# Performance work log

Hardware: AMD Instinct MI355X
Metric: run time of the kernel (lower is better)

## Reference

```python
import jax, jax.numpy as jnp
import numpy as np

B, S, T = 64, 128, 64
V, E, H, L = 32000, 512, 512, 2
PAD, BOS = 0, 1


def setup_inputs() -> dict:
    key = jax.random.key(0)
    ks = jax.random.split(key, 14)
    w = lambda k, shape: (jax.random.normal(k, shape, jnp.float32) * 0.05)
    src_emb = w(ks[0], (V, E)).at[PAD].set(0.0)
    tgt_emb = w(ks[1], (V, E)).at[PAD].set(0.0)
    enc_Wih = w(ks[2], (L, 4 * H, E))
    enc_Whh = w(ks[3], (L, 4 * H, H))
    enc_b = w(ks[4], (L, 4 * H))          # b_ih + b_hh fused
    dec_Wih = w(ks[5], (L, 4 * H, E))
    dec_Whh = w(ks[6], (L, 4 * H, H))
    dec_b = w(ks[7], (L, 4 * H))
    gen_W = w(ks[8], (V, H))
    gen_b = jnp.zeros((V,), jnp.float32)
    x_seqs = jax.random.randint(ks[9], (B, S), 0, V, jnp.int32)
    x_len = jnp.sort(jax.random.randint(ks[10], (B,), 1, S + 1, jnp.int32))[::-1]
    y_seqs = jax.random.randint(ks[11], (B, T), 0, V, jnp.int32)
    teacher = jax.random.randint(ks[12], (T - 1,), 0, 2, jnp.int32)
    return dict(x_seqs=x_seqs, x_len=x_len, y_seqs=y_seqs, teacher=teacher,
                src_emb=src_emb, tgt_emb=tgt_emb,
                enc_Wih=enc_Wih, enc_Whh=enc_Whh, enc_b=enc_b,
                dec_Wih=dec_Wih, dec_Whh=dec_Whh, dec_b=dec_b,
                gen_W=gen_W, gen_b=gen_b)


def lstm_cell(x, h, c, Wih, Whh, b):
    # torch gate order: i, f, g, o
    g = x @ Wih.T + h @ Whh.T + b
    i, f, gg, o = jnp.split(g, 4, axis=-1)
    c2 = jax.nn.sigmoid(f) * c + jax.nn.sigmoid(i) * jnp.tanh(gg)
    h2 = jax.nn.sigmoid(o) * jnp.tanh(c2)
    return h2, c2


def encode(x_seqs, x_len, src_emb, Wih, Whh, b):
    emb = src_emb[x_seqs]                                  # [B,S,E]
    mask = jnp.arange(S)[None, :] < x_len[:, None]         # [B,S] valid steps
    inp = emb.transpose(1, 0, 2)                           # [S,B,E]
    m_t = mask.T                                           # [S,B]
    hs, cs = [], []
    for l in range(L):
        def step(carry, xs, l=l):
            h, c = carry
            xt, m = xs
            h2, c2 = lstm_cell(xt, h, c, Wih[l], Whh[l], b[l])
            m = m[:, None]
            h2 = jnp.where(m, h2, h)   # freeze state past sequence length
            c2 = jnp.where(m, c2, c)
            return (h2, c2), h2
        z = jnp.zeros((B, H), inp.dtype)
        (hT, cT), out = jax.lax.scan(step, (z, z), (inp, m_t))
        inp = out
        hs.append(hT)
        cs.append(cT)
    return jnp.stack(hs), jnp.stack(cs)                    # each [L,B,H]


def reference(x_seqs, x_len, y_seqs, teacher, src_emb, tgt_emb,
              enc_Wih, enc_Whh, enc_b, dec_Wih, dec_Whh, dec_b, gen_W, gen_b):
    h0, c0 = encode(x_seqs, x_len, src_emb, enc_Wih, enc_Whh, enc_b)

    def step(carry, xs):
        h, c, inp = carry                                  # [L,B,H],[L,B,H],[B]
        y_t, tf = xs                                       # [B], scalar flag
        x = tgt_emb[inp]                                   # [B,E]
        new_h, new_c = [], []
        for l in range(L):
            hl, cl = lstm_cell(x, h[l], c[l], dec_Wih[l], dec_Whh[l], dec_b[l])
            new_h.append(hl); new_c.append(cl)
            x = hl
        logp = jax.nn.log_softmax(x @ gen_W.T + gen_b, axis=-1)   # [B,V]
        expct = jnp.take_along_axis(logp, y_t[:, None], axis=1)[:, 0]
        pred = jnp.argmax(logp, axis=1).astype(inp.dtype)
        nxt = jnp.where(tf > 0, y_t, pred)                 # scheduled sampling
        return (jnp.stack(new_h), jnp.stack(new_c), nxt), expct

    inp0 = jnp.full((B,), BOS, jnp.int32)
    _, outp = jax.lax.scan(step, (h0, c0, inp0), (y_seqs[:, 1:].T, teacher))
    return outp.T                                          # [B, T-1]
```

## Files before the change

kernel.cpp:

```cpp
#include <hip/hip_runtime.h>
#include <hip/hip_bf16.h>
#include <cstdint>
#include <cstddef>

namespace {

constexpr int B = 64, S = 128, T = 64, V = 32000, E = 512, H = 512;
constexpr int G4 = 2048;
constexpr int TM1 = T - 1;
constexpr int CHUNK = 32;
constexpr int BH = B * H;
constexpr int NT = 128;
constexpr int NTILES = V / NT;
constexpr float MARGIN = 0.02f;
constexpr unsigned NBLK = 256;

typedef __attribute__((ext_vector_type(8))) short short8v;
typedef __attribute__((ext_vector_type(4))) float f32x4;

struct GemmSh { float As[16][68]; float Bs[16][132]; };
struct StepSh { float gs[64][17]; };
struct GenSh  { float lds[64][NT + 4]; float pv1[64][4], pv2[64][4], psum[64][4], mrow[64];
                int pi1[64][4], pi2[64][4]; };
struct RedSh  { float sM[256], sS[256], red[256]; float cV[16], rV[16]; int cI[16]; int cN, nxt; };

__device__ __forceinline__ float sigf(float x) { return 1.0f / (1.0f + expf(-x)); }

__device__ __forceinline__ void split3(float w, __hip_bfloat16& a, __hip_bfloat16& b,
                                       __hip_bfloat16& c2) {
    a = __float2bfloat16(w);
    float r = w - __bfloat162float(a);
    b = __float2bfloat16(r);
    c2 = __float2bfloat16(r - __bfloat162float(b));
}


__device__ __forceinline__ unsigned ld_coh_u32(const unsigned* p) {
    unsigned v;
    asm volatile("global_load_dword %0, %1, off sc0 sc1\n\ts_waitcnt vmcnt(0)"
                 : "=v"(v) : "v"(p) : "memory");
    return v;
}
__device__ __forceinline__ void st_coh_u32(unsigned* p, unsigned v) {
    asm volatile("global_store_dword %0, %1, off sc0 sc1" :: "v"(p), "v"(v) : "memory");
}
__device__ __forceinline__ float ld_coh_f32(const float* p) {
    float v;
    asm volatile("global_load_dword %0, %1, off sc0 sc1\n\ts_waitcnt vmcnt(0)"
                 : "=v"(v) : "v"(p));
    return v;
}
__device__ __forceinline__ void st_coh_f32(float* p, float v) {
    asm volatile("global_store_dword %0, %1, off sc0 sc1" :: "v"(p), "v"(v));
}
__device__ __forceinline__ f32x4 ld_coh_f32x4(const float* p) {
    f32x4 v;
    asm volatile("global_load_dwordx4 %0, %1, off sc0 sc1\n\ts_waitcnt vmcnt(0)"
                 : "=v"(v) : "v"(p));
    return v;
}
__device__ __forceinline__ void st_coh_b16(__hip_bfloat16* p, __hip_bfloat16 v) {
    unsigned short us; __builtin_memcpy(&us, &v, 2);
    unsigned u = us;
    asm volatile("global_store_short %0, %1, off sc0 sc1" :: "v"(p), "v"(u));
}
__device__ __forceinline__ void st_coh_b128(__hip_bfloat16* p, short8v v) {
    asm volatile("global_store_dwordx4 %0, %1, off sc0 sc1" :: "v"(p), "v"(v));
}
__device__ __forceinline__ void fence_vm() {
    asm volatile("s_waitcnt vmcnt(0)" ::: "memory");
}

__device__ __forceinline__ void ldg12(const __hip_bfloat16* p0, const __hip_bfloat16* p1,
                                      const __hip_bfloat16* p2, short8v* q)
{
    asm volatile(
        "global_load_dwordx4 %0, %12, off sc0 sc1\n\t"
        "global_load_dwordx4 %1, %12, off offset:64 sc0 sc1\n\t"
        "global_load_dwordx4 %2, %12, off offset:128 sc0 sc1\n\t"
        "global_load_dwordx4 %3, %12, off offset:192 sc0 sc1\n\t"
        "global_load_dwordx4 %4, %13, off sc0 sc1\n\t"
        "global_load_dwordx4 %5, %13, off offset:64 sc0 sc1\n\t"
        "global_load_dwordx4 %6, %13, off offset:128 sc0 sc1\n\t"
        "global_load_dwordx4 %7, %13, off offset:192 sc0 sc1\n\t"
        "global_load_dwordx4 %8, %14, off sc0 sc1\n\t"
        "global_load_dwordx4 %9, %14, off offset:64 sc0 sc1\n\t"
        "global_load_dwordx4 %10, %14, off offset:128 sc0 sc1\n\t"
        "global_load_dwordx4 %11, %14, off offset:192 sc0 sc1\n\t"
        "s_waitcnt vmcnt(0)"
        : "=&v"(q[0]), "=&v"(q[1]), "=&v"(q[2]), "=&v"(q[3]),
          "=&v"(q[4]), "=&v"(q[5]), "=&v"(q[6]), "=&v"(q[7]),
          "=&v"(q[8]), "=&v"(q[9]), "=&v"(q[10]), "=&v"(q[11])
        : "v"(p0), "v"(p1), "v"(p2));
}

__device__ __forceinline__ void ldg16(const __hip_bfloat16* p0, const __hip_bfloat16* p1,
                                      const __hip_bfloat16* p2, const __hip_bfloat16* p3,
                                      short8v* q)
{
    asm volatile(
        "global_load_dwordx4 %0, %16, off sc0 sc1\n\t"
        "global_load_dwordx4 %1, %16, off offset:64 sc0 sc1\n\t"
        "global_load_dwordx4 %2, %16, off offset:128 sc0 sc1\n\t"
        "global_load_dwordx4 %3, %16, off offset:192 sc0 sc1\n\t"
        "global_load_dwordx4 %4, %17, off sc0 sc1\n\t"
        "global_load_dwordx4 %5, %17, off offset:64 sc0 sc1\n\t"
        "global_load_dwordx4 %6, %17, off offset:128 sc0 sc1\n\t"
        "global_load_dwordx4 %7, %17, off offset:192 sc0 sc1\n\t"
        "global_load_dwordx4 %8, %18, off sc0 sc1\n\t"
        "global_load_dwordx4 %9, %18, off offset:64 sc0 sc1\n\t"
        "global_load_dwordx4 %10, %18, off offset:128 sc0 sc1\n\t"
        "global_load_dwordx4 %11, %18, off offset:192 sc0 sc1\n\t"
        "global_load_dwordx4 %12, %19, off sc0 sc1\n\t"
        "global_load_dwordx4 %13, %19, off offset:64 sc0 sc1\n\t"
        "global_load_dwordx4 %14, %19, off offset:128 sc0 sc1\n\t"
        "global_load_dwordx4 %15, %19, off offset:192 sc0 sc1\n\t"
        "s_waitcnt vmcnt(0)"
        : "=&v"(q[0]), "=&v"(q[1]), "=&v"(q[2]), "=&v"(q[3]),
          "=&v"(q[4]), "=&v"(q[5]), "=&v"(q[6]), "=&v"(q[7]),
          "=&v"(q[8]), "=&v"(q[9]), "=&v"(q[10]), "=&v"(q[11]),
          "=&v"(q[12]), "=&v"(q[13]), "=&v"(q[14]), "=&v"(q[15])
        : "v"(p0), "v"(p1), "v"(p2), "v"(p3));
}

__device__ __forceinline__ void ldg8(const __hip_bfloat16* p0, const __hip_bfloat16* p1,
                                     short8v* q)
{
    asm volatile(
        "global_load_dwordx4 %0, %8, off sc0 sc1\n\t"
        "global_load_dwordx4 %1, %8, off offset:64 sc0 sc1\n\t"
        "global_load_dwordx4 %2, %8, off offset:128 sc0 sc1\n\t"
        "global_load_dwordx4 %3, %8, off offset:192 sc0 sc1\n\t"
        "global_load_dwordx4 %4, %9, off sc0 sc1\n\t"
        "global_load_dwordx4 %5, %9, off offset:64 sc0 sc1\n\t"
        "global_load_dwordx4 %6, %9, off offset:128 sc0 sc1\n\t"
        "global_load_dwordx4 %7, %9, off offset:192 sc0 sc1\n\t"
        "s_waitcnt vmcnt(0)"
        : "=&v"(q[0]), "=&v"(q[1]), "=&v"(q[2]), "=&v"(q[3]),
          "=&v"(q[4]), "=&v"(q[5]), "=&v"(q[6]), "=&v"(q[7])
        : "v"(p0), "v"(p1));
}

__device__ __forceinline__ void gbar(unsigned* flags, unsigned* gen, unsigned& ep)
{
    unsigned tgt = ++ep;
    fence_vm();
    __syncthreads();
    if (blockIdx.x == 0) {
        int tid = threadIdx.x;
        if (tid > 0) {
            int guard = 0;
            while (ld_coh_u32(&flags[tid * 32]) < tgt) {
                __builtin_amdgcn_s_sleep(2);
                if (++guard > (1 << 18)) break;
            }
        }
        __syncthreads();
        if (tid == 0) st_coh_u32(gen, tgt);
    } else {
        if (threadIdx.x == 0) {
            st_coh_u32(&flags[blockIdx.x * 32], tgt);
            int guard = 0;
            while (ld_coh_u32(gen) < tgt) {
                __builtin_amdgcn_s_sleep(2);
                if (++guard > (1 << 18)) break;
            }
        }
        __syncthreads();
    }
}

__global__ __launch_bounds__(256)
void split_dec_k(const float* __restrict__ Wih, const float* __restrict__ Whh,
                 const float* __restrict__ bsrc,
                 __hip_bfloat16* __restrict__ P0, __hip_bfloat16* __restrict__ P1,
                 __hip_bfloat16* __restrict__ P2, float* __restrict__ bint)
{
    int row = blockIdx.x;
    int l = row >> 11, jp = row & 2047;
    int kh = jp >> 2, g = jp & 3, src = g * 512 + kh;
    const float* wih = Wih + ((size_t)l * 2048 + src) * 512;
    const float* whh = Whh + ((size_t)l * 2048 + src) * 512;
    size_t ro = (size_t)row * 1024;
    for (int k = threadIdx.x; k < 1024; k += 256) {
        float w = (k < 512) ? whh[k] : wih[k - 512];
        __hip_bfloat16 a, b, c2; split3(w, a, b, c2);
        P0[ro + k] = a; P1[ro + k] = b; P2[ro + k] = c2;
    }
    if (threadIdx.x == 0) bint[row] = bsrc[l * 2048 + src];
}

__global__ __launch_bounds__(256)
void split_enc_k(const float* __restrict__ Whh,
                 __hip_bfloat16* __restrict__ P0, __hip_bfloat16* __restrict__ P1,
                 __hip_bfloat16* __restrict__ P2)
{
    int row = blockIdx.x;
    int kh = row >> 2, g = row & 3, src = g * 512 + kh;
    const float* whh = Whh + (size_t)src * 512;
    size_t ro = (size_t)row * 512;
    for (int k = threadIdx.x; k < 512; k += 256) {
        __hip_bfloat16 a, b, c2; split3(whh[k], a, b, c2);
        P0[ro + k] = a; P1[ro + k] = b; P2[ro + k] = c2;
    }
}

__device__ void gemm_tile(char* shraw, const float* __restrict__ A,
                          const float* __restrict__ Wt, const float* __restrict__ bias,
                          float* __restrict__ C,
                          const int* __restrict__ xseq, int m0, int bx, int by)
{
    GemmSh* sh = reinterpret_cast<GemmSh*>(shraw);
    constexpr int K = 512, BK = 16;
    int tid = threadIdx.x;
    int bm = by * 64, bn = bx * 128;
    int tx = tid & 15, ty = tid >> 4;
    float acc[4][8] = {};

    int lm = tid >> 2, lk = (tid & 3) << 2;
    const float* Arow;
    {
        int mg = m0 + bm + lm; int tt = mg >> 6, b = mg & 63;
        Arow = A + (size_t)xseq[b * S + tt] * K;
    }
    int ln = tid >> 1, lkb = (tid & 1) << 3;
    const float* Brow = Wt + (size_t)(bn + ln) * K;

    for (int k0 = 0; k0 < K; k0 += BK) {
        float4 av = *(const float4*)(Arow + k0 + lk);
        sh->As[lk + 0][lm] = av.x; sh->As[lk + 1][lm] = av.y;
        sh->As[lk + 2][lm] = av.z; sh->As[lk + 3][lm] = av.w;
        float4 bv0 = *(const float4*)(Brow + k0 + lkb);
        float4 bv1 = *(const float4*)(Brow + k0 + lkb + 4);
        sh->Bs[lkb + 0][ln] = bv0.x; sh->Bs[lkb + 1][ln] = bv0.y;
        sh->Bs[lkb + 2][ln] = bv0.z; sh->Bs[lkb + 3][ln] = bv0.w;
        sh->Bs[lkb + 4][ln] = bv1.x; sh->Bs[lkb + 5][ln] = bv1.y;
        sh->Bs[lkb + 6][ln] = bv1.z; sh->Bs[lkb + 7][ln] = bv1.w;
        __syncthreads();
#pragma unroll
        for (int kk = 0; kk < BK; ++kk) {
            const float4 a4  = *(const float4*)&sh->As[kk][ty * 4];
            const float4 b4a = *(const float4*)&sh->Bs[kk][tx * 8];
            const float4 b4b = *(const float4*)&sh->Bs[kk][tx * 8 + 4];
            const float a[4]  = {a4.x, a4.y, a4.z, a4.w};
            const float bb[8] = {b4a.x, b4a.y, b4a.z, b4a.w,
                                 b4b.x, b4b.y, b4b.z, b4b.w};
#pragma unroll
            for (int i = 0; i < 4; ++i)
#pragma unroll
                for (int j = 0; j < 8; ++j)
                    acc[i][j] = fmaf(a[i], bb[j], acc[i][j]);
        }
        __syncthreads();
    }
#pragma unroll
    for (int i = 0; i < 4; ++i) {
        size_t crow = (size_t)(bm + ty * 4 + i) * G4;
#pragma unroll
        for (int j = 0; j < 8; ++j) {
            int cg = bn + tx * 8 + j;
            int jp = ((cg & 511) << 2) | (cg >> 9);
            st_coh_f32(C + crow + jp, acc[i][j] + bias[cg]);
        }
    }
}

template<int KHALF, bool ADDXC, bool MASK>
__device__ void step_body(char* shraw, int blk,
    const __hip_bfloat16* __restrict__ hA0, const __hip_bfloat16* __restrict__ hA1,
    const __hip_bfloat16* __restrict__ hA2,
    const __hip_bfloat16* __restrict__ xA0, const __hip_bfloat16* __restrict__ xA1,
    const __hip_bfloat16* __restrict__ xA2,
    const __hip_bfloat16* __restrict__ W0, const __hip_bfloat16* __restrict__ W1,
    const __hip_bfloat16* __restrict__ W2,
    const float* __restrict__ addsrc, const float* __restrict__ h_in,
    float* __restrict__ h_out, float* __restrict__ c,
    __hip_bfloat16* __restrict__ o0, __hip_bfloat16* __restrict__ o1,
    __hip_bfloat16* __restrict__ o2,
    const int* __restrict__ x_len, int t)
{
    StepSh* sh = reinterpret_cast<StepSh*>(shraw);
    int tid = threadIdx.x;
    int wave = tid >> 6, lane = tid & 63;
    int lr = lane & 15, kg = (lane >> 4) * 8;
    int arow = wave * 16 + lr;
    int brow = blk * 16 + lr;
    const int KW = 512 * KHALF;

    f32x4 acc0 = {0,0,0,0}, acc1 = {0,0,0,0}, acc2 = {0,0,0,0};
    const size_t aoff = (size_t)arow * 512 + kg;
    const size_t boff = (size_t)brow * KW + kg;

#pragma unroll
    for (int g = 0; g < KHALF * 4; ++g) {
        const __hip_bfloat16 *A0, *A1, *A2; size_t go;
        if (KHALF == 2 && g >= 4) { A0 = xA0; A1 = xA1; A2 = xA2;
                                    go = aoff + (size_t)(g - 4) * 128; }
        else                      { A0 = hA0; A1 = hA1; A2 = hA2;
                                    go = aoff + (size_t)g * 128; }
        short8v q[12];
        ldg12(A0 + go, A1 + go, A2 + go, q);
#pragma unroll
        for (int j = 0; j < 4; ++j) {
            int k0 = g * 128 + j * 32;
            short8v b0 = *(const short8v*)(W0 + boff + k0);
            short8v b1 = *(const short8v*)(W1 + boff + k0);
            short8v b2 = *(const short8v*)(W2 + boff + k0);
            short8v a0 = q[j], a1 = q[4 + j], a2 = q[8 + j];
            acc0 = __builtin_amdgcn_mfma_f32_16x16x32_bf16(a0, b0, acc0, 0, 0, 0);
            acc1 = __builtin_amdgcn_mfma_f32_16x16x32_bf16(a0, b1, acc1, 0, 0, 0);
            acc2 = __builtin_amdgcn_mfma_f32_16x16x32_bf16(a1, b0, acc2, 0, 0, 0);
            acc0 = __builtin_amdgcn_mfma_f32_16x16x32_bf16(a1, b1, acc0, 0, 0, 0);
            acc1 = __builtin_amdgcn_mfma_f32_16x16x32_bf16(a0, b2, acc1, 0, 0, 0);
            acc2 = __builtin_amdgcn_mfma_f32_16x16x32_bf16(a2, b0, acc2, 0, 0, 0);
        }
    }
    int rb = (lane >> 4) * 4;
#pragma unroll
    for (int r = 0; r < 4; ++r)
        sh->gs[wave * 16 + rb + r][lr] = acc0[r] + acc1[r] + acc2[r];
    __syncthreads();

    int b = tid >> 2, khl = tid & 3;
    int khg = blk * 4 + khl;
    f32x4 add;
    if (ADDXC) add = ld_coh_f32x4(addsrc + (size_t)b * G4 + (size_t)khg * 4);
    else       add = *(const f32x4*)(addsrc + (size_t)khg * 4);
    float gi = sh->gs[b][khl * 4 + 0] + add[0];
    float gf = sh->gs[b][khl * 4 + 1] + add[1];
    float gg = sh->gs[b][khl * 4 + 2] + add[2];
    float go2 = sh->gs[b][khl * 4 + 3] + add[3];
    size_t idx = (size_t)b * H + khg;
    float cold = ld_coh_f32(c + idx);
    float c2 = sigf(gf) * cold + sigf(gi) * tanhf(gg);
    float h2 = sigf(go2) * tanhf(c2);
    if (MASK) {
        bool mk = t < x_len[b];
        if (!mk) { h2 = ld_coh_f32(h_in + idx); c2 = cold; }
    }
    if (h_out) st_coh_f32(h_out + idx, h2);
    st_coh_f32(c + idx, c2);
    __hip_bfloat16 s0, s1, s2; split3(h2, s0, s1, s2);
    st_coh_b16(o0 + idx, s0); st_coh_b16(o1 + idx, s1); st_coh_b16(o2 + idx, s2);
}

__device__ void gen_body(char* shraw, int bid,
                         const __hip_bfloat16* __restrict__ hbf,
                         const __hip_bfloat16* __restrict__ Wbf,
                         const float* __restrict__ genb,
                         float* __restrict__ part)
{
    GenSh* sh = reinterpret_cast<GenSh*>(shraw);
    int tid = threadIdx.x;
    int wave = tid >> 6, lane = tid & 63;
    int n0 = bid * NT;
    int lr = lane & 15;
    int kg = (lane >> 4) * 8;

    f32x4 acc[4][2];
    const f32x4 zero = {0.f, 0.f, 0.f, 0.f};
#pragma unroll
    for (int i = 0; i < 4; ++i)
#pragma unroll
        for (int j = 0; j < 2; ++j) acc[i][j] = zero;

    const __hip_bfloat16* Arow = hbf + (size_t)lr * 512 + kg;
    const __hip_bfloat16* Brow = Wbf + (size_t)(n0 + wave * 32 + lr) * 512 + kg;
#pragma unroll
    for (int g = 0; g < 4; ++g) {
        short8v qa[16], qb[8];
        ldg16(Arow + g * 128, Arow + 8192 + g * 128,
              Arow + 16384 + g * 128, Arow + 24576 + g * 128, qa);
        ldg8(Brow + g * 128, Brow + 8192 + g * 128, qb);
#pragma unroll
        for (int j = 0; j < 4; ++j) {
#pragma unroll
            for (int mf = 0; mf < 4; ++mf)
#pragma unroll
                for (int nf = 0; nf < 2; ++nf)
                    acc[mf][nf] = __builtin_amdgcn_mfma_f32_16x16x32_bf16(
                        qa[mf * 4 + j], qb[nf * 4 + j], acc[mf][nf], 0, 0, 0);
        }
    }
#pragma unroll
    for (int nf = 0; nf < 2; ++nf) {
        int colLocal = wave * 32 + nf * 16 + lr;
        float bias = genb[n0 + colLocal];
#pragma unroll
        for (int mf = 0; mf < 4; ++mf) {
#pragma unroll
            for (int r = 0; r < 4; ++r) {
                int row = mf * 16 + (lane >> 4) * 4 + r;
                sh->lds[row][colLocal] = acc[mf][nf][r] + bias;
            }
        }
    }
    __syncthreads();

    int row = tid >> 2, q = tid & 3;
    int cbase = q * 32;
    float v1 = -3.4e38f, v2 = -3.4e38f; int i1 = 0x7fffffff, i2 = 0x7fffffff;
    for (int c = 0; c < 32; ++c) {
        float v = sh->lds[row][cbase + c];
        int ci = cbase + c;
        if (v > v1 || (v == v1 && ci < i1)) { v2 = v1; i2 = i1; v1 = v; i1 = ci; }
        else if (v > v2 || (v == v2 && ci < i2)) { v2 = v; i2 = ci; }
    }
    sh->pv1[row][q] = v1; sh->pi1[row][q] = i1; sh->pv2[row][q] = v2; sh->pi2[row][q] = i2;
    __syncthreads();

    float t1 = -3.4e38f, t2 = -3.4e38f; int j1 = 0x7fffffff, j2 = 0x7fffffff;
    if (q == 0) {
        for (int k = 0; k < 4; ++k) {
            float a1 = sh->pv1[row][k]; int a1i = sh->pi1[row][k];
            float a2 = sh->pv2[row][k]; int a2i = sh->pi2[row][k];
            if (a1 > t1 || (a1 == t1 && a1i < j1)) { t2 = t1; j2 = j1; t1 = a1; j1 = a1i; }
            else if (a1 > t2 || (a1 == t2 && a1i < j2)) { t2 = a1; j2 = a1i; }
            if (a2 > t1 || (a2 == t1 && a2i < j1)) { t2 = t1; j2 = j1; t1 = a2; j1 = a2i; }
            else if (a2 > t2 || (a2 == t2 && a2i < j2)) { t2 = a2; j2 = a2i; }
        }
        sh->mrow[row] = t1;
    }
    __syncthreads();
    float m = sh->mrow[row];
    float s = 0.f;
    for (int c = 0; c < 32; ++c) s += expf(sh->lds[row][cbase + c] - m);
    sh->psum[row][q] = s;
    __syncthreads();
    if (q == 0) {
        float sum = sh->psum[row][0] + sh->psum[row][1] + sh->psum[row][2] + sh->psum[row][3];
        float* p = part + ((size_t)bid * B + row) * 6;
        st_coh_f32(p + 0, t1);
        st_coh_f32(p + 1, t2);
        st_coh_u32((unsigned*)(p + 2), (unsigned)(n0 + j1));
        st_coh_u32((unsigned*)(p + 3), (unsigned)(n0 + j2));
        st_coh_f32(p + 4, sum);
    }
}

__device__ void reduce_body(char* shraw, int b,
                            const float* __restrict__ part,
                            const float* __restrict__ h,
                            const float* __restrict__ genW, const float* __restrict__ genb,
                            const float* __restrict__ tgt_emb,
                            const int* __restrict__ y_seqs, const int* __restrict__ teacher,
                            float* __restrict__ outp,
                            __hip_bfloat16* __restrict__ xp0, __hip_bfloat16* __restrict__ xp1,
                            __hip_bfloat16* __restrict__ xp2, int t)
{
    RedSh* sh = reinterpret_cast<RedSh*>(shraw);
    int tid = threadIdx.x;
    int y = y_seqs[b * T + t + 1];
    const float* hrow = h + (size_t)b * 512;
    float h_a = ld_coh_f32(hrow + tid);
    float h_b = ld_coh_f32(hrow + tid + 256);

    float p_top1 = -3.4e38f, p_top2 = -3.4e38f, p_sum = 0.f;
    int p_i1 = 0x7fffffff, p_i2 = 0x7fffffff;
    if (tid < NTILES) {
        const float* p = part + ((size_t)tid * B + b) * 6;
        f32x4 v4 = ld_coh_f32x4(p);
        p_top1 = v4[0]; p_top2 = v4[1];
        p_i1 = __float_as_int(v4[2]);
        p_i2 = __float_as_int(v4[3]);
        p_sum = ld_coh_f32(p + 4);
    }
    sh->sM[tid] = p_top1; __syncthreads();
    for (int o = 128; o; o >>= 1) { if (tid < o) sh->sM[tid] = fmaxf(sh->sM[tid], sh->sM[tid + o]); __syncthreads(); }
    float M = sh->sM[0];
    if (tid == 0) sh->cN = 0;
    __syncthreads();

    float Ssum = (tid < NTILES) ? p_sum * expf(p_top1 - M) : 0.f;
    if (tid < NTILES) {
        if (p_top1 >= M - MARGIN) { int j = atomicAdd(&sh->cN, 1); if (j < 16) { sh->cV[j] = p_top1; sh->cI[j] = p_i1; } }
        if (p_top2 >= M - MARGIN) { int j = atomicAdd(&sh->cN, 1); if (j < 16) { sh->cV[j] = p_top2; sh->cI[j] = p_i2; } }
    }
    sh->sS[tid] = Ssum; __syncthreads();
    for (int o = 128; o; o >>= 1) { if (tid < o) sh->sS[tid] += sh->sS[tid + o]; __syncthreads(); }
    float lse = M + logf(sh->sS[0]);
    int nc = sh->cN < 16 ? sh->cN : 16;

    {
        const float* wrow = genW + (size_t)y * 512;
        float s = fmaf(h_a, wrow[tid], 0.f) + h_b * wrow[tid + 256];
        sh->red[tid] = s; __syncthreads();
        for (int o = 128; o; o >>= 1) { if (tid < o) sh->red[tid] += sh->red[tid + o]; __syncthreads(); }
        if (tid == 0) outp[b * TM1 + t] = sh->red[0] + genb[y] - lse;
        __syncthreads();
    }
    if (nc > 1) {
        for (int j = 0; j < nc; ++j) {
            const float* wrow = genW + (size_t)sh->cI[j] * 512;
            float s = fmaf(h_a, wrow[tid], 0.f) + h_b * wrow[tid + 256];
            sh->red[tid] = s; __syncthreads();
            for (int o = 128; o; o >>= 1) { if (tid < o) sh->red[tid] += sh->red[tid + o]; __syncthreads(); }
            if (tid == 0) sh->rV[j] = sh->red[0] + genb[sh->cI[j]];
            __syncthreads();
        }
    }
    if (tid == 0) {
        int winner;
        if (nc == 1) winner = sh->cI[0];
        else {
            float bv = -3.4e38f; int bi = 0x7fffffff;
            for (int j = 0; j < nc; ++j)
                if (sh->rV[j] > bv || (sh->rV[j] == bv && sh->cI[j] < bi)) { bv = sh->rV[j]; bi = sh->cI[j]; }
            winner = bi;
        }
        sh->nxt = (teacher[t] > 0) ? y : winner;
    }
    __syncthreads();
    int tok = sh->nxt;
    for (int k = tid; k < 512; k += 256) {
        float w = tgt_emb[(size_t)tok * 512 + k];
        __hip_bfloat16 s0, s1, s2; split3(w, s0, s1, s2);
        st_coh_b16(xp0 + (size_t)b * 512 + k, s0);
        st_coh_b16(xp1 + (size_t)b * 512 + k, s1);
        st_coh_b16(xp2 + (size_t)b * 512 + k, s2);
    }
}

struct Args {
    const int *x_seqs, *x_len, *y_seqs, *teacher;
    const float *src_emb, *tgt_emb, *eWih, *eb, *genW, *genb;
    float* Xc;
    const __hip_bfloat16 *eP0, *eP1, *eP2;
    const __hip_bfloat16 *e1P0, *e1P1, *e1P2;
    const float* ebint;
    const __hip_bfloat16 *dP0, *dP1, *dP2;
    const float* bint;
    float *hf32, *cbuf, *dech1;
    __hip_bfloat16 *P, *xP, *Wbf;
    float* part;
    float* outp;
    unsigned *flags, *gen;
};

__global__ __launch_bounds__(256, 1)
void persist_k(Args a)
{
    __shared__ __align__(16) char shpool[40960];
    unsigned ep = 0;
    const int bid = blockIdx.x;
    const int tid = threadIdx.x;
    const int gtid = bid * 256 + tid;
    const int GS = NBLK * 256;

    auto Pl = [&](int l, int slot, int pl) {
        return a.P + (((size_t)(l * 2 + slot)) * 3 + pl) * BH; };

    for (int i = gtid; i < BH; i += GS) {
        st_coh_f32(a.hf32 + i, 0.f); st_coh_f32(a.hf32 + 2 * BH + i, 0.f);
        st_coh_f32(a.cbuf + i, 0.f); st_coh_f32(a.cbuf + BH + i, 0.f);
    }
    {
        unsigned* p0 = (unsigned*)Pl(0, 0, 0);
        unsigned* p1 = (unsigned*)Pl(1, 0, 0);
        for (int i = gtid; i < 3 * BH / 2; i += GS) { st_coh_u32(p0 + i, 0u); st_coh_u32(p1 + i, 0u); }
    }
    gbar(a.flags, a.gen, ep);

    for (int c0 = 0; c0 < S; c0 += CHUNK) {
        for (int tile = bid; tile < 512; tile += NBLK)
            gemm_tile(shpool, a.src_emb, a.eWih, a.eb, a.Xc,
                      a.x_seqs, c0 * B, tile & 15, tile >> 4);
        gbar(a.flags, a.gen, ep);
        for (int tl = 0; tl < CHUNK; ++tl) {
            int t = c0 + tl;
            if (bid < 128) {
                step_body<1, true, true>(shpool, bid,
                    Pl(0, t & 1, 0), Pl(0, t & 1, 1), Pl(0, t & 1, 2),
                    nullptr, nullptr, nullptr,
                    a.eP0, a.eP1, a.eP2,
                    a.Xc + (size_t)tl * B * G4,
                    a.hf32 + (size_t)(t & 1) * BH, a.hf32 + (size_t)((t + 1) & 1) * BH,
                    a.cbuf,
                    Pl(0, (t + 1) & 1, 0), Pl(0, (t + 1) & 1, 1), Pl(0, (t + 1) & 1, 2),
                    a.x_len, t);
            } else if (t >= 1) {
                int u = t - 1;
                step_body<2, false, true>(shpool, bid - 128,
                    Pl(1, u & 1, 0), Pl(1, u & 1, 1), Pl(1, u & 1, 2),
                    Pl(0, t & 1, 0), Pl(0, t & 1, 1), Pl(0, t & 1, 2),
                    a.e1P0, a.e1P1, a.e1P2,
                    a.ebint,
                    a.hf32 + (size_t)(2 + (u & 1)) * BH, a.hf32 + (size_t)(2 + ((u + 1) & 1)) * BH,
                    a.cbuf + BH,
                    Pl(1, (u + 1) & 1, 0), Pl(1, (u + 1) & 1, 1), Pl(1, (u + 1) & 1, 2),
                    a.x_len, u);
            }
            gbar(a.flags, a.gen, ep);
        }
    }
    if (bid < 128) {
        int u = S - 1;
        step_body<2, false, true>(shpool, bid,
            Pl(1, u & 1, 0), Pl(1, u & 1, 1), Pl(1, u & 1, 2),
            Pl(0, (u + 1) & 1, 0), Pl(0, (u + 1) & 1, 1), Pl(0, (u + 1) & 1, 2),
            a.e1P0, a.e1P1, a.e1P2,
            a.ebint,
            a.hf32 + (size_t)(2 + (u & 1)) * BH, a.hf32 + (size_t)(2 + ((u + 1) & 1)) * BH,
            a.cbuf + BH,
            Pl(1, (u + 1) & 1, 0), Pl(1, (u + 1) & 1, 1), Pl(1, (u + 1) & 1, 2),
            a.x_len, u);
    }
    gbar(a.flags, a.gen, ep);

    {
        const int N8 = V * E / 8;
        for (int i = gtid; i < N8; i += GS) {
            float4 x = *(const float4*)(a.genW + (size_t)i * 8);
            float4 y = *(const float4*)(a.genW + (size_t)i * 8 + 4);
            __hip_bfloat16 tmp[8];
            tmp[0] = __float2bfloat16(x.x); tmp[1] = __float2bfloat16(x.y);
            tmp[2] = __float2bfloat16(x.z); tmp[3] = __float2bfloat16(x.w);
            tmp[4] = __float2bfloat16(y.x); tmp[5] = __float2bfloat16(y.y);
            tmp[6] = __float2bfloat16(y.z); tmp[7] = __float2bfloat16(y.w);
            st_coh_b128(a.Wbf + (size_t)i * 8, *(const short8v*)tmp);
        }
        for (int i = gtid; i < BH; i += GS) {
            int k = i & 511;
            float w = a.tgt_emb[512 + k];
            __hip_bfloat16 s0, s1, s2; split3(w, s0, s1, s2);
            st_coh_b16(a.xP + i, s0);
            st_coh_b16(a.xP + BH + i, s1);
            st_coh_b16(a.xP + 2 * BH + i, s2);
        }
    }
    gbar(a.flags, a.gen, ep);

    for (int t = 0; t < TM1; ++t) {
        int si = t & 1, so = si ^ 1;
        if (bid < 128)
            step_body<2, false, false>(shpool, bid,
                Pl(0, si, 0), Pl(0, si, 1), Pl(0, si, 2),
                a.xP, a.xP + BH, a.xP + 2 * BH,
                a.dP0, a.dP1, a.dP2, a.bint,
                nullptr, nullptr, a.cbuf,
                Pl(0, so, 0), Pl(0, so, 1), Pl(0, so, 2),
                nullptr, 0);
        gbar(a.flags, a.gen, ep);
        if (bid < 128)
            step_body<2, false, false>(shpool, bid,
                Pl(1, si, 0), Pl(1, si, 1), Pl(1, si, 2),
                Pl(0, so, 0), Pl(0, so, 1), Pl(0, so, 2),
                a.dP0 + (size_t)G4 * 1024, a.dP1 + (size_t)G4 * 1024,
                a.dP2 + (size_t)G4 * 1024, a.bint + G4,
                nullptr, a.dech1, a.cbuf + BH,
                Pl(1, so, 0), Pl(1, so, 1), Pl(1, so, 2),
                nullptr, 0);
        gbar(a.flags, a.gen, ep);
        if (bid < NTILES)
            gen_body(shpool, bid, Pl(1, so, 0), a.Wbf, a.genb, a.part);
        gbar(a.flags, a.gen, ep);
        if (bid < B)
            reduce_body(shpool, bid, a.part, a.dech1, a.genW, a.genb, a.tgt_emb,
                        a.y_seqs, a.teacher, a.outp,
                        a.xP, a.xP + BH, a.xP + 2 * BH, t);
        gbar(a.flags, a.gen, ep);
    }
}

}

extern "C" void kernel_launch(void* const* d_in, const int* in_sizes, int n_in,
                              void* d_out, int out_size, void* d_ws, size_t ws_size,
                              hipStream_t stream)
{
    (void)in_sizes; (void)n_in; (void)out_size;
    const int*   x_seqs  = (const int*)  d_in[0];
    const int*   x_len   = (const int*)  d_in[1];
    const int*   y_seqs  = (const int*)  d_in[2];
    const int*   teacher = (const int*)  d_in[3];
    const float* src_emb = (const float*)d_in[4];
    const float* tgt_emb = (const float*)d_in[5];
    const float* eWih    = (const float*)d_in[6];
    const float* eWhh    = (const float*)d_in[7];
    const float* eb      = (const float*)d_in[8];
    const float* dWih    = (const float*)d_in[9];
    const float* dWhh    = (const float*)d_in[10];
    const float* db      = (const float*)d_in[11];
    const float* genW    = (const float*)d_in[12];
    const float* genb    = (const float*)d_in[13];

    float* w = (float*)d_ws;
    size_t off = 0;
    auto take = [&](size_t n) { float* p = w + off; off += n; return p; };
    auto takeb = [&](size_t n) { return (__hip_bfloat16*)take((n + 1) / 2); };

    unsigned* flags = (unsigned*)take(256 * 32 + 32);
    float* Xc = take((size_t)CHUNK * B * G4);
    __hip_bfloat16* eP0  = takeb((size_t)G4 * 512);
    __hip_bfloat16* eP1  = takeb((size_t)G4 * 512);
    __hip_bfloat16* eP2  = takeb((size_t)G4 * 512);
    __hip_bfloat16* e1P0 = takeb((size_t)G4 * 1024);
    __hip_bfloat16* e1P1 = takeb((size_t)G4 * 1024);
    __hip_bfloat16* e1P2 = takeb((size_t)G4 * 1024);
    float* ebint = take((size_t)G4);
    __hip_bfloat16* dP0 = takeb((size_t)2 * G4 * 1024);
    __hip_bfloat16* dP1 = takeb((size_t)2 * G4 * 1024);
    __hip_bfloat16* dP2 = takeb((size_t)2 * G4 * 1024);
    float* bint  = take(2 * (size_t)G4);
    float* hf32  = take(4 * (size_t)BH);
    float* cbuf  = take(2 * (size_t)BH);
    float* dech1 = take((size_t)BH);
    __hip_bfloat16* P  = takeb((size_t)12 * BH);
    __hip_bfloat16* xP = takeb((size_t)3 * BH);
    float* part_f = take((size_t)NTILES * B * 6);
    if (ws_size < off * sizeof(float)) return;

    dim3 tpb256(256);
    split_enc_k<<<dim3(G4), tpb256, 0, stream>>>(eWhh, eP0, eP1, eP2);
    split_dec_k<<<dim3(G4), tpb256, 0, stream>>>(
        eWih + (size_t)G4 * E, eWhh + (size_t)G4 * E, eb + G4, e1P0, e1P1, e1P2, ebint);
    split_dec_k<<<dim3(2 * G4), tpb256, 0, stream>>>(
        dWih, dWhh, db, dP0, dP1, dP2, bint);
    hipError_t _e = hipMemsetAsync(flags, 0, (256 * 32 + 32) * sizeof(unsigned), stream);
    (void)_e;

    Args a;
    a.x_seqs = x_seqs; a.x_len = x_len; a.y_seqs = y_seqs; a.teacher = teacher;
    a.src_emb = src_emb; a.tgt_emb = tgt_emb; a.eWih = eWih; a.eb = eb;
    a.genW = genW; a.genb = genb;
    a.Xc = Xc;
    a.eP0 = eP0; a.eP1 = eP1; a.eP2 = eP2;
    a.e1P0 = e1P0; a.e1P1 = e1P1; a.e1P2 = e1P2; a.ebint = ebint;
    a.dP0 = dP0; a.dP1 = dP1; a.dP2 = dP2; a.bint = bint;
    a.hf32 = hf32; a.cbuf = cbuf; a.dech1 = dech1;
    a.P = P; a.xP = xP;
    a.Wbf = (__hip_bfloat16*)Xc;
    a.part = part_f;
    a.outp = (float*)d_out;
    a.flags = flags; a.gen = flags + 256 * 32;

    persist_k<<<dim3(NBLK), tpb256, 0, stream>>>(a);
}
```

Baseline: 10.25 ms.

## Double-buffer A-operand loads, widen LSTM step tiles, and use per-block barrier release flags

```diff
diff --git a/kernel.cpp b/kernel.cpp
--- a/kernel.cpp
+++ b/kernel.cpp
@@ -19,7 +19,7 @@
 typedef __attribute__((ext_vector_type(4))) float f32x4;
 
 struct GemmSh { float As[16][68]; float Bs[16][132]; };
-struct StepSh { float gs[64][17]; };
+struct StepSh { float gs[64][33]; };
 struct GenSh  { float lds[64][NT + 4]; float pv1[64][4], pv2[64][4], psum[64][4], mrow[64];
                 int pi1[64][4], pi2[64][4]; };
 struct RedSh  { float sM[256], sS[256], red[256]; float cV[16], rV[16]; int cI[16]; int cN, nxt; };
@@ -34,7 +34,6 @@
     c2 = __float2bfloat16(r - __bfloat162float(b));
 }
 
-
 __device__ __forceinline__ unsigned ld_coh_u32(const unsigned* p) {
     unsigned v;
     asm volatile("global_load_dword %0, %1, off sc0 sc1\n\ts_waitcnt vmcnt(0)"
@@ -71,8 +70,8 @@
     asm volatile("s_waitcnt vmcnt(0)" ::: "memory");
 }
 
-__device__ __forceinline__ void ldg12(const __hip_bfloat16* p0, const __hip_bfloat16* p1,
-                                      const __hip_bfloat16* p2, short8v* q)
+__device__ __forceinline__ void issue12(const __hip_bfloat16* p0, const __hip_bfloat16* p1,
+                                        const __hip_bfloat16* p2, short8v* q)
 {
     asm volatile(
         "global_load_dwordx4 %0, %12, off sc0 sc1\n\t"
@@ -86,17 +85,15 @@
         "global_load_dwordx4 %8, %14, off sc0 sc1\n\t"
         "global_load_dwordx4 %9, %14, off offset:64 sc0 sc1\n\t"
         "global_load_dwordx4 %10, %14, off offset:128 sc0 sc1\n\t"
-        "global_load_dwordx4 %11, %14, off offset:192 sc0 sc1\n\t"
-        "s_waitcnt vmcnt(0)"
+        "global_load_dwordx4 %11, %14, off offset:192 sc0 sc1"
         : "=&v"(q[0]), "=&v"(q[1]), "=&v"(q[2]), "=&v"(q[3]),
           "=&v"(q[4]), "=&v"(q[5]), "=&v"(q[6]), "=&v"(q[7]),
           "=&v"(q[8]), "=&v"(q[9]), "=&v"(q[10]), "=&v"(q[11])
         : "v"(p0), "v"(p1), "v"(p2));
 }
-
-__device__ __forceinline__ void ldg16(const __hip_bfloat16* p0, const __hip_bfloat16* p1,
-                                      const __hip_bfloat16* p2, const __hip_bfloat16* p3,
-                                      short8v* q)
+__device__ __forceinline__ void issue16(const __hip_bfloat16* p0, const __hip_bfloat16* p1,
+                                        const __hip_bfloat16* p2, const __hip_bfloat16* p3,
+                                        short8v* q)
 {
     asm volatile(
         "global_load_dwordx4 %0, %16, off sc0 sc1\n\t"
@@ -114,40 +111,33 @@
         "global_load_dwordx4 %12, %19, off sc0 sc1\n\t"
         "global_load_dwordx4 %13, %19, off offset:64 sc0 sc1\n\t"
         "global_load_dwordx4 %14, %19, off offset:128 sc0 sc1\n\t"
-        "global_load_dwordx4 %15, %19, off offset:192 sc0 sc1\n\t"
-        "s_waitcnt vmcnt(0)"
+        "global_load_dwordx4 %15, %19, off offset:192 sc0 sc1"
         : "=&v"(q[0]), "=&v"(q[1]), "=&v"(q[2]), "=&v"(q[3]),
           "=&v"(q[4]), "=&v"(q[5]), "=&v"(q[6]), "=&v"(q[7]),
           "=&v"(q[8]), "=&v"(q[9]), "=&v"(q[10]), "=&v"(q[11]),
           "=&v"(q[12]), "=&v"(q[13]), "=&v"(q[14]), "=&v"(q[15])
         : "v"(p0), "v"(p1), "v"(p2), "v"(p3));
 }
-
-__device__ __forceinline__ void ldg8(const __hip_bfloat16* p0, const __hip_bfloat16* p1,
-                                     short8v* q)
-{
-    asm volatile(
-        "global_load_dwordx4 %0, %8, off sc0 sc1\n\t"
-        "global_load_dwordx4 %1, %8, off offset:64 sc0 sc1\n\t"
-        "global_load_dwordx4 %2, %8, off offset:128 sc0 sc1\n\t"
-        "global_load_dwordx4 %3, %8, off offset:192 sc0 sc1\n\t"
-        "global_load_dwordx4 %4, %9, off sc0 sc1\n\t"
-        "global_load_dwordx4 %5, %9, off offset:64 sc0 sc1\n\t"
-        "global_load_dwordx4 %6, %9, off offset:128 sc0 sc1\n\t"
-        "global_load_dwordx4 %7, %9, off offset:192 sc0 sc1\n\t"
-        "s_waitcnt vmcnt(0)"
-        : "=&v"(q[0]), "=&v"(q[1]), "=&v"(q[2]), "=&v"(q[3]),
-          "=&v"(q[4]), "=&v"(q[5]), "=&v"(q[6]), "=&v"(q[7])
-        : "v"(p0), "v"(p1));
-}
-
-__device__ __forceinline__ void gbar(unsigned* flags, unsigned* gen, unsigned& ep)
+__device__ __forceinline__ void wait_vm12() {
+    asm volatile("s_waitcnt vmcnt(12)" ::: "memory");
+    __builtin_amdgcn_sched_barrier(0);
+}
+__device__ __forceinline__ void wait_vm16() {
+    asm volatile("s_waitcnt vmcnt(16)" ::: "memory");
+    __builtin_amdgcn_sched_barrier(0);
+}
+__device__ __forceinline__ void wait_vm0s() {
+    asm volatile("s_waitcnt vmcnt(0)" ::: "memory");
+    __builtin_amdgcn_sched_barrier(0);
+}
+
+__device__ __forceinline__ void gbar(unsigned* flags, unsigned* rel, unsigned& ep)
 {
     unsigned tgt = ++ep;
     fence_vm();
     __syncthreads();
+    const int tid = threadIdx.x;
     if (blockIdx.x == 0) {
-        int tid = threadIdx.x;
         if (tid > 0) {
             int guard = 0;
             while (ld_coh_u32(&flags[tid * 32]) < tgt) {
@@ -156,12 +146,12 @@
             }
         }
         __syncthreads();
-        if (tid == 0) st_coh_u32(gen, tgt);
+        st_coh_u32(&rel[tid * 32], tgt);
     } else {
-        if (threadIdx.x == 0) {
+        if (tid == 0) {
             st_coh_u32(&flags[blockIdx.x * 32], tgt);
             int guard = 0;
-            while (ld_coh_u32(gen) < tgt) {
+            while (ld_coh_u32(&rel[blockIdx.x * 32]) < tgt) {
                 __builtin_amdgcn_s_sleep(2);
                 if (++guard > (1 << 18)) break;
             }
@@ -284,64 +274,96 @@
     int wave = tid >> 6, lane = tid & 63;
     int lr = lane & 15, kg = (lane >> 4) * 8;
     int arow = wave * 16 + lr;
-    int brow = blk * 16 + lr;
     const int KW = 512 * KHALF;
-
-    f32x4 acc0 = {0,0,0,0}, acc1 = {0,0,0,0}, acc2 = {0,0,0,0};
     const size_t aoff = (size_t)arow * 512 + kg;
-    const size_t boff = (size_t)brow * KW + kg;
-
-#pragma unroll
-    for (int g = 0; g < KHALF * 4; ++g) {
-        const __hip_bfloat16 *A0, *A1, *A2; size_t go;
-        if (KHALF == 2 && g >= 4) { A0 = xA0; A1 = xA1; A2 = xA2;
-                                    go = aoff + (size_t)(g - 4) * 128; }
-        else                      { A0 = hA0; A1 = hA1; A2 = hA2;
-                                    go = aoff + (size_t)g * 128; }
-        short8v q[12];
-        ldg12(A0 + go, A1 + go, A2 + go, q);
+    const size_t boff0 = (size_t)(blk * 32 + lr) * KW + kg;
+    const size_t boff1 = (size_t)(blk * 32 + 16 + lr) * KW + kg;
+    constexpr int NG = KHALF * 4;
+
+    f32x4 a00 = {0,0,0,0}, a01 = {0,0,0,0}, a02 = {0,0,0,0};
+    f32x4 a10 = {0,0,0,0}, a11 = {0,0,0,0}, a12 = {0,0,0,0};
+
+    auto ap = [&](int g, int pl) -> const __hip_bfloat16* {
+        const __hip_bfloat16* base;
+        if (KHALF == 2 && g >= 4) {
+            base = (pl == 0) ? xA0 : (pl == 1) ? xA1 : xA2;
+            return base + aoff + (size_t)(g - 4) * 128;
+        }
+        base = (pl == 0) ? hA0 : (pl == 1) ? hA1 : hA2;
+        return base + aoff + (size_t)g * 128;
+    };
+
+    short8v qa[2][12];
+    issue12(ap(0, 0), ap(0, 1), ap(0, 2), qa[0]);
+#pragma unroll
+    for (int g = 0; g < NG; ++g) {
+        if (g + 1 < NG) {
+            issue12(ap(g + 1, 0), ap(g + 1, 1), ap(g + 1, 2), qa[(g + 1) & 1]);
+            wait_vm12();
+        } else {
+            wait_vm0s();
+        }
 #pragma unroll
         for (int j = 0; j < 4; ++j) {
             int k0 = g * 128 + j * 32;
-            short8v b0 = *(const short8v*)(W0 + boff + k0);
-            short8v b1 = *(const short8v*)(W1 + boff + k0);
-            short8v b2 = *(const short8v*)(W2 + boff + k0);
-            short8v a0 = q[j], a1 = q[4 + j], a2 = q[8 + j];
-            acc0 = __builtin_amdgcn_mfma_f32_16x16x32_bf16(a0, b0, acc0, 0, 0, 0);
-            acc1 = __builtin_amdgcn_mfma_f32_16x16x32_bf16(a0, b1, acc1, 0, 0, 0);
-            acc2 = __builtin_amdgcn_mfma_f32_16x16x32_bf16(a1, b0, acc2, 0, 0, 0);
-            acc0 = __builtin_amdgcn_mfma_f32_16x16x32_bf16(a1, b1, acc0, 0, 0, 0);
-            acc1 = __builtin_amdgcn_mfma_f32_16x16x32_bf16(a0, b2, acc1, 0, 0, 0);
-            acc2 = __builtin_amdgcn_mfma_f32_16x16x32_bf16(a2, b0, acc2, 0, 0, 0);
+            short8v a0 = qa[g & 1][j], a1 = qa[g & 1][4 + j], a2 = qa[g & 1][8 + j];
+            {
+                short8v b0 = *(const short8v*)(W0 + boff0 + k0);
+                short8v b1 = *(const short8v*)(W1 + boff0 + k0);
+                short8v b2 = *(const short8v*)(W2 + boff0 + k0);
+                a00 = __builtin_amdgcn_mfma_f32_16x16x32_bf16(a0, b0, a00, 0, 0, 0);
+                a01 = __builtin_amdgcn_mfma_f32_16x16x32_bf16(a0, b1, a01, 0, 0, 0);
+                a02 = __builtin_amdgcn_mfma_f32_16x16x32_bf16(a1, b0, a02, 0, 0, 0);
+                a00 = __builtin_amdgcn_mfma_f32_16x16x32_bf16(a1, b1, a00, 0, 0, 0);
+                a01 = __builtin_amdgcn_mfma_f32_16x16x32_bf16(a0, b2, a01, 0, 0, 0);
+                a02 = __builtin_amdgcn_mfma_f32_16x16x32_bf16(a2, b0, a02, 0, 0, 0);
+            }
+            {
+                short8v b0 = *(const short8v*)(W0 + boff1 + k0);
+                short8v b1 = *(const short8v*)(W1 + boff1 + k0);
+                short8v b2 = *(const short8v*)(W2 + boff1 + k0);
+                a10 = __builtin_amdgcn_mfma_f32_16x16x32_bf16(a0, b0, a10, 0, 0, 0);
+                a11 = __builtin_amdgcn_mfma_f32_16x16x32_bf16(a0, b1, a11, 0, 0, 0);
+                a12 = __builtin_amdgcn_mfma_f32_16x16x32_bf16(a1, b0, a12, 0, 0, 0);
+                a10 = __builtin_amdgcn_mfma_f32_16x16x32_bf16(a1, b1, a10, 0, 0, 0);
+                a11 = __builtin_amdgcn_mfma_f32_16x16x32_bf16(a0, b2, a11, 0, 0, 0);
+                a12 = __builtin_amdgcn_mfma_f32_16x16x32_bf16(a2, b0, a12, 0, 0, 0);
+            }
         }
     }
     int rb = (lane >> 4) * 4;
 #pragma unroll
-    for (int r = 0; r < 4; ++r)
-        sh->gs[wave * 16 + rb + r][lr] = acc0[r] + acc1[r] + acc2[r];
+    for (int r = 0; r < 4; ++r) {
+        sh->gs[wave * 16 + rb + r][lr]      = a00[r] + a01[r] + a02[r];
+        sh->gs[wave * 16 + rb + r][16 + lr] = a10[r] + a11[r] + a12[r];
+    }
     __syncthreads();
 
-    int b = tid >> 2, khl = tid & 3;
-    int khg = blk * 4 + khl;
-    f32x4 add;
-    if (ADDXC) add = ld_coh_f32x4(addsrc + (size_t)b * G4 + (size_t)khg * 4);
-    else       add = *(const f32x4*)(addsrc + (size_t)khg * 4);
-    float gi = sh->gs[b][khl * 4 + 0] + add[0];
-    float gf = sh->gs[b][khl * 4 + 1] + add[1];
-    float gg = sh->gs[b][khl * 4 + 2] + add[2];
-    float go2 = sh->gs[b][khl * 4 + 3] + add[3];
-    size_t idx = (size_t)b * H + khg;
-    float cold = ld_coh_f32(c + idx);
-    float c2 = sigf(gf) * cold + sigf(gi) * tanhf(gg);
-    float h2 = sigf(go2) * tanhf(c2);
-    if (MASK) {
-        bool mk = t < x_len[b];
-        if (!mk) { h2 = ld_coh_f32(h_in + idx); c2 = cold; }
-    }
-    if (h_out) st_coh_f32(h_out + idx, h2);
-    st_coh_f32(c + idx, c2);
-    __hip_bfloat16 s0, s1, s2; split3(h2, s0, s1, s2);
-    st_coh_b16(o0 + idx, s0); st_coh_b16(o1 + idx, s1); st_coh_b16(o2 + idx, s2);
+    int b = tid >> 2, q4 = tid & 3;
+#pragma unroll
+    for (int kk = 0; kk < 2; ++kk) {
+        int kh_l = q4 + kk * 4;
+        int khg = blk * 8 + kh_l;
+        f32x4 add;
+        if (ADDXC) add = ld_coh_f32x4(addsrc + (size_t)b * G4 + (size_t)khg * 4);
+        else       add = *(const f32x4*)(addsrc + (size_t)khg * 4);
+        float gi  = sh->gs[b][kh_l * 4 + 0] + add[0];
+        float gf  = sh->gs[b][kh_l * 4 + 1] + add[1];
+        float gg  = sh->gs[b][kh_l * 4 + 2] + add[2];
+        float go2 = sh->gs[b][kh_l * 4 + 3] + add[3];
+        size_t idx = (size_t)b * H + khg;
+        float cold = ld_coh_f32(c + idx);
+        float c2 = sigf(gf) * cold + sigf(gi) * tanhf(gg);
+        float h2 = sigf(go2) * tanhf(c2);
+        if (MASK) {
+            bool mk = t < x_len[b];
+            if (!mk) { h2 = ld_coh_f32(h_in + idx); c2 = cold; }
+        }
+        if (h_out) st_coh_f32(h_out + idx, h2);
+        st_coh_f32(c + idx, c2);
+        __hip_bfloat16 s0, s1, s2; split3(h2, s0, s1, s2);
+        st_coh_b16(o0 + idx, s0); st_coh_b16(o1 + idx, s1); st_coh_b16(o2 + idx, s2);
+    }
 }
 
 __device__ void gen_body(char* shraw, int bid,
@@ -366,20 +388,29 @@
 
     const __hip_bfloat16* Arow = hbf + (size_t)lr * 512 + kg;
     const __hip_bfloat16* Brow = Wbf + (size_t)(n0 + wave * 32 + lr) * 512 + kg;
+
+    short8v qa[2][16];
+    issue16(Arow, Arow + 8192, Arow + 16384, Arow + 24576, qa[0]);
 #pragma unroll
     for (int g = 0; g < 4; ++g) {
-        short8v qa[16], qb[8];
-        ldg16(Arow + g * 128, Arow + 8192 + g * 128,
-              Arow + 16384 + g * 128, Arow + 24576 + g * 128, qa);
-        ldg8(Brow + g * 128, Brow + 8192 + g * 128, qb);
+        if (g < 3) {
+            issue16(Arow + (g + 1) * 128, Arow + 8192 + (g + 1) * 128,
+                    Arow + 16384 + (g + 1) * 128, Arow + 24576 + (g + 1) * 128,
+                    qa[(g + 1) & 1]);
+            wait_vm16();
+        } else {
+            wait_vm0s();
+        }
 #pragma unroll
         for (int j = 0; j < 4; ++j) {
 #pragma unroll
-            for (int mf = 0; mf < 4; ++mf)
-#pragma unroll
-                for (int nf = 0; nf < 2; ++nf)
+            for (int nf = 0; nf < 2; ++nf) {
+                short8v bb = *(const short8v*)(Brow + (size_t)nf * 8192 + g * 128 + j * 32);
+#pragma unroll
+                for (int mf = 0; mf < 4; ++mf)
                     acc[mf][nf] = __builtin_amdgcn_mfma_f32_16x16x32_bf16(
-                        qa[mf * 4 + j], qb[nf * 4 + j], acc[mf][nf], 0, 0, 0);
+                        qa[g & 1][mf * 4 + j], bb, acc[mf][nf], 0, 0, 0);
+            }
         }
     }
 #pragma unroll
@@ -534,7 +565,7 @@
     __hip_bfloat16 *P, *xP, *Wbf;
     float* part;
     float* outp;
-    unsigned *flags, *gen;
+    unsigned *flags, *rel;
 };
 
 __global__ __launch_bounds__(256, 1)
@@ -559,16 +590,16 @@
         unsigned* p1 = (unsigned*)Pl(1, 0, 0);
         for (int i = gtid; i < 3 * BH / 2; i += GS) { st_coh_u32(p0 + i, 0u); st_coh_u32(p1 + i, 0u); }
     }
-    gbar(a.flags, a.gen, ep);
+    gbar(a.flags, a.rel, ep);
 
     for (int c0 = 0; c0 < S; c0 += CHUNK) {
         for (int tile = bid; tile < 512; tile += NBLK)
             gemm_tile(shpool, a.src_emb, a.eWih, a.eb, a.Xc,
                       a.x_seqs, c0 * B, tile & 15, tile >> 4);
-        gbar(a.flags, a.gen, ep);
+        gbar(a.flags, a.rel, ep);
         for (int tl = 0; tl < CHUNK; ++tl) {
             int t = c0 + tl;
-            if (bid < 128) {
+            if (bid < 64) {
                 step_body<1, true, true>(shpool, bid,
                     Pl(0, t & 1, 0), Pl(0, t & 1, 1), Pl(0, t & 1, 2),
                     nullptr, nullptr, nullptr,
@@ -578,9 +609,9 @@
                     a.cbuf,
                     Pl(0, (t + 1) & 1, 0), Pl(0, (t + 1) & 1, 1), Pl(0, (t + 1) & 1, 2),
                     a.x_len, t);
-            } else if (t >= 1) {
+            } else if (bid < 128 && t >= 1) {
                 int u = t - 1;
-                step_body<2, false, true>(shpool, bid - 128,
+                step_body<2, false, true>(shpool, bid - 64,
                     Pl(1, u & 1, 0), Pl(1, u & 1, 1), Pl(1, u & 1, 2),
                     Pl(0, t & 1, 0), Pl(0, t & 1, 1), Pl(0, t & 1, 2),
                     a.e1P0, a.e1P1, a.e1P2,
@@ -590,10 +621,10 @@
                     Pl(1, (u + 1) & 1, 0), Pl(1, (u + 1) & 1, 1), Pl(1, (u + 1) & 1, 2),
                     a.x_len, u);
             }
-            gbar(a.flags, a.gen, ep);
-        }
-    }
-    if (bid < 128) {
+            gbar(a.flags, a.rel, ep);
+        }
+    }
+    if (bid < 64) {
         int u = S - 1;
         step_body<2, false, true>(shpool, bid,
             Pl(1, u & 1, 0), Pl(1, u & 1, 1), Pl(1, u & 1, 2),
@@ -605,7 +636,10 @@
             Pl(1, (u + 1) & 1, 0), Pl(1, (u + 1) & 1, 1), Pl(1, (u + 1) & 1, 2),
             a.x_len, u);
     }
-    gbar(a.flags, a.gen, ep);
+    gbar(a.flags, a.rel, ep);
+
+    __builtin_amdgcn_fence(__ATOMIC_RELEASE, "agent");
+    gbar(a.flags, a.rel, ep);
 
     {
         const int N8 = V * E / 8;
@@ -628,11 +662,12 @@
             st_coh_b16(a.xP + 2 * BH + i, s2);
         }
     }
-    gbar(a.flags, a.gen, ep);
+    __builtin_amdgcn_fence(__ATOMIC_ACQUIRE, "agent");
+    gbar(a.flags, a.rel, ep);
 
     for (int t = 0; t < TM1; ++t) {
         int si = t & 1, so = si ^ 1;
-        if (bid < 128)
+        if (bid < 64)
             step_body<2, false, false>(shpool, bid,
                 Pl(0, si, 0), Pl(0, si, 1), Pl(0, si, 2),
                 a.xP, a.xP + BH, a.xP + 2 * BH,
@@ -640,8 +675,8 @@
                 nullptr, nullptr, a.cbuf,
                 Pl(0, so, 0), Pl(0, so, 1), Pl(0, so, 2),
                 nullptr, 0);
-        gbar(a.flags, a.gen, ep);
-        if (bid < 128)
+        gbar(a.flags, a.rel, ep);
+        if (bid < 64)
             step_body<2, false, false>(shpool, bid,
                 Pl(1, si, 0), Pl(1, si, 1), Pl(1, si, 2),
                 Pl(0, so, 0), Pl(0, so, 1), Pl(0, so, 2),
@@ -650,15 +685,15 @@
                 nullptr, a.dech1, a.cbuf + BH,
                 Pl(1, so, 0), Pl(1, so, 1), Pl(1, so, 2),
                 nullptr, 0);
-        gbar(a.flags, a.gen, ep);
+        gbar(a.flags, a.rel, ep);
         if (bid < NTILES)
             gen_body(shpool, bid, Pl(1, so, 0), a.Wbf, a.genb, a.part);
-        gbar(a.flags, a.gen, ep);
+        gbar(a.flags, a.rel, ep);
         if (bid < B)
             reduce_body(shpool, bid, a.part, a.dech1, a.genW, a.genb, a.tgt_emb,
                         a.y_seqs, a.teacher, a.outp,
                         a.xP, a.xP + BH, a.xP + 2 * BH, t);
-        gbar(a.flags, a.gen, ep);
+        gbar(a.flags, a.rel, ep);
     }
 }
 
@@ -689,7 +724,8 @@
     auto take = [&](size_t n) { float* p = w + off; off += n; return p; };
     auto takeb = [&](size_t n) { return (__hip_bfloat16*)take((n + 1) / 2); };
 
-    unsigned* flags = (unsigned*)take(256 * 32 + 32);
+    unsigned* flags = (unsigned*)take(256 * 32);
+    unsigned* rel   = (unsigned*)take(256 * 32);
     float* Xc = take((size_t)CHUNK * B * G4);
     __hip_bfloat16* eP0  = takeb((size_t)G4 * 512);
     __hip_bfloat16* eP1  = takeb((size_t)G4 * 512);
@@ -716,7 +752,7 @@
         eWih + (size_t)G4 * E, eWhh + (size_t)G4 * E, eb + G4, e1P0, e1P1, e1P2, ebint);
     split_dec_k<<<dim3(2 * G4), tpb256, 0, stream>>>(
         dWih, dWhh, db, dP0, dP1, dP2, bint);
-    hipError_t _e = hipMemsetAsync(flags, 0, (256 * 32 + 32) * sizeof(unsigned), stream);
+    hipError_t _e = hipMemsetAsync(flags, 0, 2 * 256 * 32 * sizeof(unsigned), stream);
     (void)_e;
 
     Args a;
@@ -732,7 +768,7 @@
     a.Wbf = (__hip_bfloat16*)Xc;
     a.part = part_f;
     a.outp = (float*)d_out;
-    a.flags = flags; a.gen = flags + 256 * 32;
+    a.flags = flags; a.rel = rel;
 
     persist_k<<<dim3(NBLK), tpb256, 0, stream>>>(a);
 }
```

Result: slower. 13.56 ms (+32.3%).
